# Kernel tuning notes

Hardware: AMD Instinct MI355X
Metric: run time of the kernel (lower is better)

## Reference

```python
import jax, jax.numpy as jnp
import numpy as np

K = 9            # box-filter size per axis
PAD = (K - 1) // 2
KSIZE = K * K * K  # 729


def _box_sum(x):
    """Separable 9x9x9 box sum with zero padding (same math as conv3d with all-ones kernel)."""
    for i in range(3):  # loop over the 3 spatial axes (fixed small structural loop)
        ks = [1, 1, 1]
        ks[i] = K
        pad = [(0, 0)] * 3
        pad[i] = (PAD, PAD)
        kern = jnp.ones((1, 1, *ks), x.dtype)
        x = jax.lax.conv_general_dilated(
            x, kern, window_strides=(1, 1, 1), padding=pad,
            dimension_numbers=('NCDHW', 'OIDHW', 'NCDHW'))
    return x


def setup_inputs() -> dict:
    key = jax.random.key(0)
    k1, k2 = jax.random.split(key)
    shape = (2, 1, 160, 192, 160)
    return {
        'input': jax.random.normal(k1, shape, dtype=jnp.float32),
        'target': jax.random.normal(k2, shape, dtype=jnp.float32),
    }


def reference(input, target):
    # target rescaled from (-1, 1) to (0, 1), as in the torch module
    target = (target + 1.0) * 0.5

    II = input * input
    TT = target * target
    IT = input * target

    T_sum = _box_sum(target)
    I_sum = _box_sum(input)
    TT_sum = _box_sum(TT)
    II_sum = _box_sum(II)
    IT_sum = _box_sum(IT)

    Ihat = I_sum / KSIZE
    That = T_sum / KSIZE

    cross = IT_sum - Ihat * T_sum - That * I_sum + That * Ihat * KSIZE
    T_var = TT_sum - 2.0 * That * T_sum + That * That * KSIZE
    I_var = II_sum - 2.0 * Ihat * I_sum + Ihat * Ihat * KSIZE

    cc = cross * cross / (T_var * I_var + 1e-5)
    return -1.0 * jnp.mean(cc)
```

## Files before the change

kernel.cpp:

```cpp
#include <hip/hip_runtime.h>

namespace {

typedef _Float16 half_t;
typedef _Float16 half2_t __attribute__((ext_vector_type(2)));
typedef _Float16 half4_t __attribute__((ext_vector_type(4)));

constexpr int Wd = 160, Hd = 192, Dd = 160;
constexpr int TX = 16, TY = 16, CZ = 40;
constexpr int HW = Hd * Wd;
constexpr int LIVE = CZ + 8;
constexpr float INV_K = 1.0f / 729.0f;
constexpr float INV_TOT = 1.0f / 9830400.0f;
constexpr int R4 = 17;
constexpr int RTH = 68;
constexpr int ROWS = 26;


__global__ __launch_bounds__(256, 4)
void ncc_main(const float* __restrict__ inp, const float* __restrict__ tgt,
              float* __restrict__ out)
{
    __shared__ half4_t xs4h[2][ROWS * R4];
    __shared__ half_t  xsTh[2][ROWS * RTH];
    __shared__ float   red[4];

    const int tid = threadIdx.x;
    const int n  = (int)blockIdx.z >> 2;
    const int zc = (int)blockIdx.z & 3;
    const int x0 = blockIdx.x * TX, y0 = blockIdx.y * TY, z0 = zc * CZ;

    const int f = tid % 5;
    const int j = tid / 5;
    const int r = j >> 1, h = j & 1;
    const int gy = y0 - 4 + r;
    const bool yok = (tid < 240) && (gy >= 0) && (gy < Hd);
    const int gyc = min(max(gy, 0), Hd - 1);
    const int gxb = x0 - 4 + 8 * h;
    const bool uI = (f == 0) || (f == 1) || (f == 3);
    const float bI = (f == 0) ? 1.f : 0.f;
    const float bT = (f == 1 || f == 2) ? 0.5f : 0.f;
    const float bC = (f == 1 || f == 2) ? 0.5f : ((f >= 3) ? 1.f : 0.f);

#define DECODE(c) \
    int voff##c; float aI##c, aTC##c; \
    { const int gx = gxb + 4 * c; \
      const float m = (yok && gx >= 0 && gx < Wd) ? 1.f : 0.f; \
      const int gxc = min(max(gx, 0), Wd - 4); \
      voff##c = gyc * Wd + gxc; \
      aI##c = uI ? m : 0.f; aTC##c = uI ? 0.f : 0.5f * m; }
    DECODE(0) DECODE(1) DECODE(2) DECODE(3)
#undef DECODE

    const int nb = n * (Dd * HW);
    const float* baseI = inp + nb;
    const float* baseT = tgt + nb;

    const int stoff = (f < 4) ? ((r * R4) * 4 + 32 * h + f) : (r * RTH + 32 * h);
    half_t* const st0 = (f < 4) ? ((half_t*)xs4h[0] + stoff) : (xsTh[0] + stoff);
    half_t* const st1 = (f < 4) ? ((half_t*)xs4h[1] + stoff) : (xsTh[1] + stoff);

    const int yi = tid >> 4, xi = tid & 15;
    const half4_t* const rd4_0 = &xs4h[0][yi * R4 + xi];
    const half4_t* const rd4_1 = &xs4h[1][yi * R4 + xi];
    const half_t*  const rdT_0 = &xsTh[0][yi * RTH + 4 * xi];
    const half_t*  const rdT_1 = &xsTh[1][yi * RTH + 4 * xi];

    const half2_t hz = {(half_t)0.f, (half_t)0.f};
    half2_t R01_0=hz,R01_1=hz,R01_2=hz,R01_3=hz,R01_4=hz,R01_5=hz,R01_6=hz,R01_7=hz,R01_8=hz;
    half2_t R23_0=hz,R23_1=hz,R23_2=hz,R23_3=hz,R23_4=hz,R23_5=hz,R23_6=hz,R23_7=hz,R23_8=hz;
    float   RT_0=0.f,RT_1=0.f,RT_2=0.f,RT_3=0.f,RT_4=0.f,RT_5=0.f,RT_6=0.f,RT_7=0.f,RT_8=0.f;
    float4 S4 = make_float4(0.f, 0.f, 0.f, 0.f);
    float ST = 0.f, acc = 0.f;

    float4 Ic0, Ic1, Ic2, Ic3, Tc0, Tc1, Tc2, Tc3;
    Ic0 = Ic1 = Ic2 = Ic3 = make_float4(0.f, 0.f, 0.f, 0.f);
    Tc0 = Tc1 = Tc2 = Tc3 = Ic0;

#define PRELOAD(zz) { \
    const float* pI = baseI + (zz) * HW; \
    const float* pT = baseT + (zz) * HW; \
    Ic0 = *(const float4*)(pI + voff0); Tc0 = *(const float4*)(pT + voff0); \
    Ic1 = *(const float4*)(pI + voff1); Tc1 = *(const float4*)(pT + voff1); \
    Ic2 = *(const float4*)(pI + voff2); Tc2 = *(const float4*)(pT + voff2); \
    Ic3 = *(const float4*)(pI + voff3); Tc3 = *(const float4*)(pT + voff3); }

    if (z0 - 4 >= 0) PRELOAD(z0 - 4)

#define PRODC(c, P0, P1, P2, P3) { \
    P0 = fmaf(Ic##c.x, aI##c, fmaf(Tc##c.x, aTC##c, aTC##c)) * fmaf(Ic##c.x, bI, fmaf(Tc##c.x, bT, bC)); \
    P1 = fmaf(Ic##c.y, aI##c, fmaf(Tc##c.y, aTC##c, aTC##c)) * fmaf(Ic##c.y, bI, fmaf(Tc##c.y, bT, bC)); \
    P2 = fmaf(Ic##c.z, aI##c, fmaf(Tc##c.z, aTC##c, aTC##c)) * fmaf(Ic##c.z, bI, fmaf(Tc##c.z, bT, bC)); \
    P3 = fmaf(Ic##c.w, aI##c, fmaf(Tc##c.w, aTC##c, aTC##c)) * fmaf(Ic##c.w, bI, fmaf(Tc##c.w, bT, bC)); }

#define SHIFT9(P, NV) \
    P##_0 = P##_1; P##_1 = P##_2; P##_2 = P##_3; P##_3 = P##_4; P##_4 = P##_5; \
    P##_5 = P##_6; P##_6 = P##_7; P##_7 = P##_8; P##_8 = (NV);

    for (int tb = 0; tb < 54; tb += 18) {
        #pragma unroll
        for (int u = 0; u < 18; ++u) {
            const int s = tb + u;
            if (s < LIVE) {
                const int zi = z0 - 4 + s;
                const bool zok = (zi >= 0) && (zi < Dd);
                const int pb = u & 1;

                float p0, p1, p2, p3, p4, p5, p6, p7, p8, p9, p10, p11, p12, p13, p14, p15;
                if (zok) {
                    PRODC(0, p0,  p1,  p2,  p3)
                    PRODC(1, p4,  p5,  p6,  p7)
                    PRODC(2, p8,  p9,  p10, p11)
                    PRODC(3, p12, p13, p14, p15)
                }

                {
                    const int zi2 = z0 - 3 + s;
                    if ((s + 1) < LIVE && zi2 >= 0 && zi2 < Dd) PRELOAD(zi2)
                }

                if (zok) {
                    half_t* const st = pb ? st1 : st0;
                    float ss = p0 + p1 + p2 + p3 + p4 + p5 + p6 + p7 + p8;
                    st[0]  = (half_t)ss;
                    ss += p9  - p0; st[4]  = (half_t)ss;
                    ss += p10 - p1; st[8]  = (half_t)ss;
                    ss += p11 - p2; st[12] = (half_t)ss;
                    ss += p12 - p3; st[16] = (half_t)ss;
                    ss += p13 - p4; st[20] = (half_t)ss;
                    ss += p14 - p5; st[24] = (half_t)ss;
                    ss += p15 - p6; st[28] = (half_t)ss;
                }

                __syncthreads();

                half2_t a01 = hz, a23 = hz;
                float aTf = 0.f;
                if (zok) {
                    const half4_t* const rd4 = pb ? rd4_1 : rd4_0;
                    const half_t*  const rdT = pb ? rdT_1 : rdT_0;
                    half_t aT = (half_t)0.f;
                    #pragma unroll
                    for (int k = 0; k < 9; ++k) {
                        const half4_t v = rd4[k * R4];
                        const half2_t vlo = {v.x, v.y};
                        const half2_t vhi = {v.z, v.w};
                        a01 += vlo; a23 += vhi;
                        aT += rdT[k * RTH];
                    }
                    aTf = (float)aT;
                }

                S4.x += (float)a01.x - (float)R01_0.x;
                S4.y += (float)a01.y - (float)R01_0.y;
                S4.z += (float)a23.x - (float)R23_0.x;
                S4.w += (float)a23.y - (float)R23_0.y;
                ST   += aTf - RT_0;
                SHIFT9(R01, a01)
                SHIFT9(R23, a23)
                SHIFT9(RT, aTf)

                if (s >= 8) {
                    const float sii = S4.x, sit = S4.y, stt = S4.z, si = S4.w, stv = ST;
                    const float cross = sit - si * stv * INV_K;
                    const float tvar  = stt - stv * stv * INV_K;
                    const float ivar  = sii - si  * si  * INV_K;
                    acc += cross * cross * __builtin_amdgcn_rcpf(tvar * ivar + 1e-5f);
                }
            }
        }
    }
#undef PRELOAD
#undef PRODC
#undef SHIFT9

    #pragma unroll
    for (int off = 32; off > 0; off >>= 1) acc += __shfl_down(acc, off, 64);
    if ((tid & 63) == 0) red[tid >> 6] = acc;
    __syncthreads();
    if (tid == 0) {
        const float tot = red[0] + red[1] + red[2] + red[3];
        atomicAdd(out, -tot * INV_TOT);
    }
}

}

extern "C" void kernel_launch(void* const* d_in, const int* in_sizes, int n_in,
                              void* d_out, int out_size, void* d_ws, size_t ws_size,
                              hipStream_t stream)
{
    const float* inp = (const float*)d_in[0];
    const float* tgt = (const float*)d_in[1];
    float* out = (float*)d_out;

    hipMemsetAsync(d_out, 0, sizeof(float), stream);
    dim3 grid(Wd / TX, Hd / TY, 2 * (Dd / CZ));
    ncc_main<<<grid, 256, 0, stream>>>(inp, tgt, out);
}
```

Before: 187.1 us.

## Deepen global prefetch to two slices and move z-history ring to LDS

Loads the input and target tiles two depth slices ahead, alternating between two register sets, so global-load latency is hidden across more iterations. The nine-slice running-sum history moves from shifted registers to a per-thread ring buffer in shared memory to free the registers the second prefetch set needs. Launch bounds drop from four to two blocks per CU. The cost is extra LDS traffic and footprint per slice and lower occupancy.

```diff
diff --git a/kernel.cpp b/kernel.cpp
--- a/kernel.cpp
+++ b/kernel.cpp
@@ -17,18 +17,26 @@
 constexpr int ROWS = 26;
 
 
-__global__ __launch_bounds__(256, 4)
+__global__ __launch_bounds__(256, 2)
 void ncc_main(const float* __restrict__ inp, const float* __restrict__ tgt,
               float* __restrict__ out)
 {
     __shared__ half4_t xs4h[2][ROWS * R4];
     __shared__ half_t  xsTh[2][ROWS * RTH];
+    __shared__ half4_t ringAB[9 * 256];
+    __shared__ half_t  ringT[9 * 256];
     __shared__ float   red[4];
 
     const int tid = threadIdx.x;
     const int n  = (int)blockIdx.z >> 2;
     const int zc = (int)blockIdx.z & 3;
     const int x0 = blockIdx.x * TX, y0 = blockIdx.y * TY, z0 = zc * CZ;
+
+    #pragma unroll
+    for (int q = 0; q < 9; ++q) {
+        ringAB[q * 256 + tid] = (half4_t)0;
+        ringT[q * 256 + tid] = (half_t)0.f;
+    }
 
     const int f = tid % 5;
     const int j = tid / 5;
@@ -66,113 +74,115 @@
     const half_t*  const rdT_0 = &xsTh[0][yi * RTH + 4 * xi];
     const half_t*  const rdT_1 = &xsTh[1][yi * RTH + 4 * xi];
 
-    const half2_t hz = {(half_t)0.f, (half_t)0.f};
-    half2_t R01_0=hz,R01_1=hz,R01_2=hz,R01_3=hz,R01_4=hz,R01_5=hz,R01_6=hz,R01_7=hz,R01_8=hz;
-    half2_t R23_0=hz,R23_1=hz,R23_2=hz,R23_3=hz,R23_4=hz,R23_5=hz,R23_6=hz,R23_7=hz,R23_8=hz;
-    float   RT_0=0.f,RT_1=0.f,RT_2=0.f,RT_3=0.f,RT_4=0.f,RT_5=0.f,RT_6=0.f,RT_7=0.f,RT_8=0.f;
     float4 S4 = make_float4(0.f, 0.f, 0.f, 0.f);
     float ST = 0.f, acc = 0.f;
 
-    float4 Ic0, Ic1, Ic2, Ic3, Tc0, Tc1, Tc2, Tc3;
-    Ic0 = Ic1 = Ic2 = Ic3 = make_float4(0.f, 0.f, 0.f, 0.f);
-    Tc0 = Tc1 = Tc2 = Tc3 = Ic0;
-
-#define PRELOAD(zz) { \
+#define DECL_SET(S) \
+    float4 S##I0, S##I1, S##I2, S##I3, S##T0, S##T1, S##T2, S##T3; \
+    S##I0 = S##I1 = S##I2 = S##I3 = make_float4(0.f, 0.f, 0.f, 0.f); \
+    S##T0 = S##T1 = S##T2 = S##T3 = S##I0;
+    DECL_SET(A) DECL_SET(B)
+#undef DECL_SET
+
+#define PRELOAD(S, zz) { \
     const float* pI = baseI + (zz) * HW; \
     const float* pT = baseT + (zz) * HW; \
-    Ic0 = *(const float4*)(pI + voff0); Tc0 = *(const float4*)(pT + voff0); \
-    Ic1 = *(const float4*)(pI + voff1); Tc1 = *(const float4*)(pT + voff1); \
-    Ic2 = *(const float4*)(pI + voff2); Tc2 = *(const float4*)(pT + voff2); \
-    Ic3 = *(const float4*)(pI + voff3); Tc3 = *(const float4*)(pT + voff3); }
-
-    if (z0 - 4 >= 0) PRELOAD(z0 - 4)
-
-#define PRODC(c, P0, P1, P2, P3) { \
-    P0 = fmaf(Ic##c.x, aI##c, fmaf(Tc##c.x, aTC##c, aTC##c)) * fmaf(Ic##c.x, bI, fmaf(Tc##c.x, bT, bC)); \
-    P1 = fmaf(Ic##c.y, aI##c, fmaf(Tc##c.y, aTC##c, aTC##c)) * fmaf(Ic##c.y, bI, fmaf(Tc##c.y, bT, bC)); \
-    P2 = fmaf(Ic##c.z, aI##c, fmaf(Tc##c.z, aTC##c, aTC##c)) * fmaf(Ic##c.z, bI, fmaf(Tc##c.z, bT, bC)); \
-    P3 = fmaf(Ic##c.w, aI##c, fmaf(Tc##c.w, aTC##c, aTC##c)) * fmaf(Ic##c.w, bI, fmaf(Tc##c.w, bT, bC)); }
-
-#define SHIFT9(P, NV) \
-    P##_0 = P##_1; P##_1 = P##_2; P##_2 = P##_3; P##_3 = P##_4; P##_4 = P##_5; \
-    P##_5 = P##_6; P##_6 = P##_7; P##_7 = P##_8; P##_8 = (NV);
+    S##I0 = *(const float4*)(pI + voff0); S##T0 = *(const float4*)(pT + voff0); \
+    S##I1 = *(const float4*)(pI + voff1); S##T1 = *(const float4*)(pT + voff1); \
+    S##I2 = *(const float4*)(pI + voff2); S##T2 = *(const float4*)(pT + voff2); \
+    S##I3 = *(const float4*)(pI + voff3); S##T3 = *(const float4*)(pT + voff3); }
+
+    if (z0 - 4 >= 0) PRELOAD(A, z0 - 4)
+    if (z0 - 3 >= 0) PRELOAD(B, z0 - 3)
+
+#define PRODC(S, c, P0, P1, P2, P3) { \
+    P0 = fmaf(S##I##c.x, aI##c, fmaf(S##T##c.x, aTC##c, aTC##c)) * fmaf(S##I##c.x, bI, fmaf(S##T##c.x, bT, bC)); \
+    P1 = fmaf(S##I##c.y, aI##c, fmaf(S##T##c.y, aTC##c, aTC##c)) * fmaf(S##I##c.y, bI, fmaf(S##T##c.y, bT, bC)); \
+    P2 = fmaf(S##I##c.z, aI##c, fmaf(S##T##c.z, aTC##c, aTC##c)) * fmaf(S##I##c.z, bI, fmaf(S##T##c.z, bT, bC)); \
+    P3 = fmaf(S##I##c.w, aI##c, fmaf(S##T##c.w, aTC##c, aTC##c)) * fmaf(S##I##c.w, bI, fmaf(S##T##c.w, bT, bC)); }
+
+#define SLICE_BODY(SET) { \
+    const int zi = z0 - 4 + s; \
+    const bool zok = (zi >= 0) && (zi < Dd);         \
+    const int sl = u % 9;                            \
+    const int pb = u & 1;                            \
+    float o0, o1, o2, o3, o4, o5, o6, o7; \
+    if (zok) { \
+        float p0, p1, p2, p3, p4, p5, p6, p7; \
+        float p8, p9, p10, p11, p12, p13, p14, p15; \
+        PRODC(SET, 0, p0,  p1,  p2,  p3) \
+        PRODC(SET, 1, p4,  p5,  p6,  p7) \
+        PRODC(SET, 2, p8,  p9,  p10, p11) \
+        PRODC(SET, 3, p12, p13, p14, p15) \
+        float ss = p0 + p1 + p2 + p3 + p4 + p5 + p6 + p7 + p8; \
+        o0 = ss; \
+        ss += p9  - p0; o1 = ss; \
+        ss += p10 - p1; o2 = ss; \
+        ss += p11 - p2; o3 = ss; \
+        ss += p12 - p3; o4 = ss; \
+        ss += p13 - p4; o5 = ss; \
+        ss += p14 - p5; o6 = ss; \
+        ss += p15 - p6; o7 = ss; \
+    } \
+    {    \
+        const int zi2 = z0 - 2 + s; \
+        if ((s + 2) < LIVE && zi2 >= 0 && zi2 < Dd) PRELOAD(SET, zi2) \
+    } \
+    if (zok) { \
+        half_t* const st = pb ? st1 : st0; \
+        st[0]  = (half_t)o0; st[4]  = (half_t)o1; \
+        st[8]  = (half_t)o2; st[12] = (half_t)o3; \
+        st[16] = (half_t)o4; st[20] = (half_t)o5; \
+        st[24] = (half_t)o6; st[28] = (half_t)o7; \
+    } \
+    __syncthreads();                                 \
+    half2_t a01 = (half2_t)0, a23 = (half2_t)0; \
+    half_t aT = (half_t)0.f; \
+    if (zok) { \
+        const half4_t* const rd4 = pb ? rd4_1 : rd4_0; \
+        const half_t*  const rdT = pb ? rdT_1 : rdT_0; \
+        _Pragma("unroll") \
+        for (int k = 0; k < 9; ++k) { \
+            const half4_t v = rd4[k * R4]; \
+            const half2_t vlo = {v.x, v.y}; \
+            const half2_t vhi = {v.z, v.w}; \
+            a01 += vlo; a23 += vhi; \
+            aT += rdT[k * RTH]; \
+        } \
+    } \
+    {    \
+        const half4_t oAB = ringAB[sl * 256 + tid]; \
+        const half_t  oT  = ringT[sl * 256 + tid]; \
+        S4.x += (float)a01.x - (float)oAB.x; \
+        S4.y += (float)a01.y - (float)oAB.y; \
+        S4.z += (float)a23.x - (float)oAB.z; \
+        S4.w += (float)a23.y - (float)oAB.w; \
+        ST   += (float)aT - (float)oT; \
+        const half4_t nAB = {a01.x, a01.y, a23.x, a23.y}; \
+        ringAB[sl * 256 + tid] = nAB; \
+        ringT[sl * 256 + tid]  = aT; \
+    } \
+    if (s >= 8) {                                    \
+        const float sii = S4.x, sit = S4.y, stt = S4.z, si = S4.w, stv = ST; \
+        const float cross = sit - si * stv * INV_K; \
+        const float tvar  = stt - stv * stv * INV_K; \
+        const float ivar  = sii - si  * si  * INV_K; \
+        acc += cross * cross * __builtin_amdgcn_rcpf(tvar * ivar + 1e-5f); \
+    } }
 
     for (int tb = 0; tb < 54; tb += 18) {
         #pragma unroll
         for (int u = 0; u < 18; ++u) {
             const int s = tb + u;
             if (s < LIVE) {
-                const int zi = z0 - 4 + s;
-                const bool zok = (zi >= 0) && (zi < Dd);
-                const int pb = u & 1;
-
-                float p0, p1, p2, p3, p4, p5, p6, p7, p8, p9, p10, p11, p12, p13, p14, p15;
-                if (zok) {
-                    PRODC(0, p0,  p1,  p2,  p3)
-                    PRODC(1, p4,  p5,  p6,  p7)
-                    PRODC(2, p8,  p9,  p10, p11)
-                    PRODC(3, p12, p13, p14, p15)
-                }
-
-                {
-                    const int zi2 = z0 - 3 + s;
-                    if ((s + 1) < LIVE && zi2 >= 0 && zi2 < Dd) PRELOAD(zi2)
-                }
-
-                if (zok) {
-                    half_t* const st = pb ? st1 : st0;
-                    float ss = p0 + p1 + p2 + p3 + p4 + p5 + p6 + p7 + p8;
-                    st[0]  = (half_t)ss;
-                    ss += p9  - p0; st[4]  = (half_t)ss;
-                    ss += p10 - p1; st[8]  = (half_t)ss;
-                    ss += p11 - p2; st[12] = (half_t)ss;
-                    ss += p12 - p3; st[16] = (half_t)ss;
-                    ss += p13 - p4; st[20] = (half_t)ss;
-                    ss += p14 - p5; st[24] = (half_t)ss;
-                    ss += p15 - p6; st[28] = (half_t)ss;
-                }
-
-                __syncthreads();
-
-                half2_t a01 = hz, a23 = hz;
-                float aTf = 0.f;
-                if (zok) {
-                    const half4_t* const rd4 = pb ? rd4_1 : rd4_0;
-                    const half_t*  const rdT = pb ? rdT_1 : rdT_0;
-                    half_t aT = (half_t)0.f;
-                    #pragma unroll
-                    for (int k = 0; k < 9; ++k) {
-                        const half4_t v = rd4[k * R4];
-                        const half2_t vlo = {v.x, v.y};
-                        const half2_t vhi = {v.z, v.w};
-                        a01 += vlo; a23 += vhi;
-                        aT += rdT[k * RTH];
-                    }
-                    aTf = (float)aT;
-                }
-
-                S4.x += (float)a01.x - (float)R01_0.x;
-                S4.y += (float)a01.y - (float)R01_0.y;
-                S4.z += (float)a23.x - (float)R23_0.x;
-                S4.w += (float)a23.y - (float)R23_0.y;
-                ST   += aTf - RT_0;
-                SHIFT9(R01, a01)
-                SHIFT9(R23, a23)
-                SHIFT9(RT, aTf)
-
-                if (s >= 8) {
-                    const float sii = S4.x, sit = S4.y, stt = S4.z, si = S4.w, stv = ST;
-                    const float cross = sit - si * stv * INV_K;
-                    const float tvar  = stt - stv * stv * INV_K;
-                    const float ivar  = sii - si  * si  * INV_K;
-                    acc += cross * cross * __builtin_amdgcn_rcpf(tvar * ivar + 1e-5f);
-                }
+                if ((u & 1) == 0) SLICE_BODY(A)
+                else              SLICE_BODY(B)
             }
         }
     }
+#undef SLICE_BODY
 #undef PRELOAD
 #undef PRODC
-#undef SHIFT9
 
     #pragma unroll
     for (int off = 32; off > 0; off >>= 1) acc += __shfl_down(acc, off, 64);
```

New measurement: 166.8 us. 1.12x faster.
